# Kernel tuning notes

Measured on AMD Instinct MI355X. Metric: run time of the kernel, lower is better.

Reference implementation:

```python
import jax, jax.numpy as jnp
import numpy as np

WIN = (2, 6, 12)          # (win_Z, win_H, win_W)
HEADS = 6
DIM = 192
IMG = (8, 96, 180)        # (Z, H, W) after patch embedding
NWIN_TOK = WIN[0] * WIN[1] * WIN[2]            # 144 tokens per window
TYPE_W = (IMG[0] // WIN[0]) * (IMG[1] // WIN[1])  # num_Z*num_H = 64
BIAS_ROWS = (2 * WIN[2] - 1) * WIN[1] ** 2 * WIN[0] ** 2  # 3312


def _build_position_index(win):
    wZ, wH, wW = win
    czi = np.arange(wZ); czj = -np.arange(wZ) * wZ
    chi = np.arange(wH); chj = -np.arange(wH) * wH
    cw = np.arange(wW)
    c1 = np.stack(np.meshgrid(czi, chi, cw, indexing='ij'), 0).reshape(3, -1)
    c2 = np.stack(np.meshgrid(czj, chj, cw, indexing='ij'), 0).reshape(3, -1)
    coords = (c1[:, :, None] - c2[:, None, :]).transpose(1, 2, 0).copy()  # (N, N, 3)
    coords[:, :, 2] += wW - 1
    coords[:, :, 1] *= 2 * wW - 1
    coords[:, :, 0] *= (2 * wW - 1) * wH ** 2
    return jnp.asarray(coords.sum(-1).reshape(-1))  # (N*N,) int indices into bias table

POS_IDX = _build_position_index(WIN)


def _layernorm(x, g, b, eps=1e-5):
    m = jnp.mean(x, -1, keepdims=True)
    v = jnp.mean(jnp.square(x - m), -1, keepdims=True)
    return (x - m) * jax.lax.rsqrt(v + eps) * g + b


def setup_inputs() -> dict:
    key = jax.random.key(0)
    ks = jax.random.split(key, 8)
    Z, H, W = IMG
    x = jax.random.normal(ks[0], (1, Z * H * W, DIM), dtype=jnp.float32)
    std = 0.02
    return {
        'x': x,
        'w_qkv': jax.random.normal(ks[1], (DIM, 3 * DIM), dtype=jnp.float32) * std,
        'b_qkv': jnp.zeros((3 * DIM,), jnp.float32),
        'w_proj': jax.random.normal(ks[2], (DIM, DIM), dtype=jnp.float32) * std,
        'b_proj': jnp.zeros((DIM,), jnp.float32),
        'bias_table': jax.random.normal(ks[3], (BIAS_ROWS, TYPE_W, HEADS), dtype=jnp.float32) * std,
        'g1': jnp.ones((DIM,), jnp.float32), 'b1': jnp.zeros((DIM,), jnp.float32),
        'g2': jnp.ones((DIM,), jnp.float32), 'b2': jnp.zeros((DIM,), jnp.float32),
        'w_mlp': jax.random.normal(ks[4], (DIM, DIM), dtype=jnp.float32) * std,
        'b_mlp': jnp.zeros((DIM,), jnp.float32),
        'Z': Z, 'H': H, 'W': W, 'roll': 0,
    }


def reference(x, w_qkv, b_qkv, w_proj, b_proj, bias_table, g1, b1, g2, b2,
              w_mlp, b_mlp, Z, H, W, roll):
    # roll=0 path (is_rolling=False, mask=None), per init_kwargs
    B, T, C = x.shape
    wZ, wH, wW = WIN
    nZ, nH, nW = Z // wZ, H // wH, W // wW
    hd = C // HEADS
    scale = float(hd) ** 0.5
    N = NWIN_TOK

    shortcut = x
    # window partition: (B,Z,H,W,C) -> (B*nZ*nH*nW, N, C)
    xw = (x.reshape(B, nZ, wZ, nH, wH, nW, wW, C)
            .transpose(0, 1, 3, 5, 2, 4, 6, 7)
            .reshape(-1, N, C))
    Bw = xw.shape[0]

    qkv = (xw @ w_qkv + b_qkv).reshape(Bw, N, 3, HEADS, hd).transpose(2, 0, 3, 1, 4)
    q, k, v = qkv[0], qkv[1], qkv[2]                       # (Bw, heads, N, hd)

    attn = jnp.einsum('bhnd,bhmd->bhnm', q, k) / scale     # (Bw, heads, N, N)

    # earth-specific relative position bias: gather then broadcast over f = Bw // TYPE_W
    bias = bias_table[POS_IDX].reshape(N, N, TYPE_W, HEADS).transpose(2, 3, 0, 1)
    f = Bw // TYPE_W
    attn = (attn.reshape(f, TYPE_W, HEADS, N, N) + bias[None]).reshape(Bw, HEADS, N, N)

    attn = jax.nn.softmax(attn, axis=-1)
    out = jnp.einsum('bhnm,bhmd->bhnd', attn, v).transpose(0, 2, 1, 3).reshape(Bw, N, C)
    out = out @ w_proj + b_proj

    # window merge back to (B, Z*H*W, C)
    out = (out.reshape(B, nZ, nH, nW, wZ, wH, wW, C)
              .transpose(0, 1, 4, 2, 5, 3, 6, 7)
              .reshape(B, Z * H * W, C))

    x = shortcut + _layernorm(out, g1, b1)
    x = x + _layernorm(x @ w_mlp + b_mlp, g2, b2)
    return x
```

## Files before the change

kernel.cpp:

```cpp
#include <hip/hip_runtime.h>
#include <hip/hip_bf16.h>


typedef __attribute__((ext_vector_type(8))) short bfrag;
typedef __attribute__((ext_vector_type(4))) float f32x4;
typedef __attribute__((ext_vector_type(4))) unsigned short us4;
typedef __attribute__((ext_vector_type(8))) unsigned short us8;

__device__ __forceinline__ unsigned short f2bf(float f) {
    __hip_bfloat16 h = __float2bfloat16(f);
    unsigned short s;
    __builtin_memcpy(&s, &h, 2);
    return s;
}
__device__ __forceinline__ us4 pack4(float a, float b, float c, float d) {
    us4 o;
    o[0] = f2bf(a); o[1] = f2bf(b); o[2] = f2bf(c); o[3] = f2bf(d);
    return o;
}
__device__ __forceinline__ float bf2f(unsigned short s) {
    return __builtin_bit_cast(float, ((unsigned int)s) << 16);
}
__device__ __forceinline__ int token_of(int iw, int n) {
    int wi = iw % 15, hi = (iw / 15) % 16, zi = iw / 240;
    int ww = n % 12, hh = (n / 12) % 6, zz = n / 72;
    return ((zi * 2 + zz) * 96 + hi * 6 + hh) * 180 + wi * 12 + ww;
}

__global__ __launch_bounds__(256) void wconv(const float* __restrict__ w_qkv,
                                             unsigned short* __restrict__ wt) {
    int id = blockIdx.x * 256 + threadIdx.x;
    if (id >= 110592) return;
    int k = id / 576, c = id - k * 576;
    wt[c * 192 + k] = f2bf(w_qkv[id]);
}

__global__ __launch_bounds__(256) void wconv2(const float* __restrict__ w_proj,
                                              const float* __restrict__ w_mlp,
                                              unsigned short* __restrict__ wp_t,
                                              unsigned short* __restrict__ wm_t) {
    int id = blockIdx.x * 256 + threadIdx.x;
    if (id >= 36864) return;
    const float* src = blockIdx.y ? w_mlp : w_proj;
    unsigned short* dst = blockIdx.y ? wm_t : wp_t;
    int n = id / 192, k = id - n * 192;
    dst[id] = f2bf(src[(size_t)k * 192 + n]);
}

__global__ __launch_bounds__(256) void bias_reorg(const float* __restrict__ bias_table,
                                                  unsigned short* __restrict__ bias_r) {
    __shared__ unsigned short T[384][68];
    int p0 = blockIdx.x * 64;
    int tid = threadIdx.x;
    for (int e = tid; e < 64 * 384; e += 256) {
        int pl = e / 384, th = e - pl * 384;
        int pair = p0 + pl;
        int i = pair / 144, j = pair - i * 144;
        int z1 = i / 72, h1 = (i / 12) % 6, w1 = i % 12;
        int z2 = j / 72, h2 = (j / 12) % 6, w2 = j % 12;
        int idx = (z1 + 2 * z2) * 828 + (h1 + 6 * h2) * 23 + (w1 - w2 + 11);
        T[th][pl] = f2bf(bias_table[(size_t)idx * 384 + th]);
    }
    __syncthreads();
    for (int e = tid; e < 384 * 16; e += 256) {
        int th = e >> 4, pc = e & 15;
        *(us4*)&bias_r[(size_t)th * 20736 + p0 + pc * 4] = *(const us4*)&T[th][pc * 4];
    }
}

__global__ __launch_bounds__(384) void qkattn(const float* __restrict__ x,
                                              const unsigned short* __restrict__ wt,
                                              const float* __restrict__ b_qkv,
                                              const unsigned short* __restrict__ bias_r,
                                              unsigned short* __restrict__ o_ws) {
    __shared__ __align__(16) unsigned short Xw[144 * 200];
    __shared__ __align__(16) unsigned short Ql[2][144 * 40];
    __shared__ __align__(16) unsigned short Kl[2][144 * 40];
    __shared__ __align__(16) unsigned short Vt[2][32 * 168];
    int tid = threadIdx.x;
    int iw = blockIdx.x;
    int w = tid >> 6, l = tid & 63, li = l & 15, lg = l >> 4;
    int tri = w / 3, tw = w - tri * 3;

#pragma unroll
    for (int i = 0; i < 9; ++i) {
        int idx = tid + i * 384;
        int r = idx / 24, g = idx - r * 24;
        const float* xp = &x[(size_t)token_of(iw, r) * 192 + g * 8];
        float4 v0 = *(const float4*)xp;
        float4 v1 = *(const float4*)(xp + 4);
        us4 a = pack4(v0.x, v0.y, v0.z, v0.w);
        us4 b = pack4(v1.x, v1.y, v1.z, v1.w);
        *(us4*)&Xw[r * 200 + g * 8] = a;
        *(us4*)&Xw[r * 200 + g * 8 + 4] = b;
    }
    __syncthreads();

    for (int rnd = 0; rnd < 3; ++rnd) {
        int h = rnd * 2 + tri;

        int wrow = tw * 192 + h * 32;
        f32x4 acc[2][9];
#pragma unroll
        for (int ct = 0; ct < 2; ++ct)
#pragma unroll
            for (int tt = 0; tt < 9; ++tt) acc[ct][tt] = (f32x4){0.f, 0.f, 0.f, 0.f};
        for (int kk = 0; kk < 6; ++kk) {
            int k0 = kk * 32 + lg * 8;
            bfrag wf[2];
#pragma unroll
            for (int ct = 0; ct < 2; ++ct)
                wf[ct] = *(const bfrag*)&wt[(size_t)(wrow + ct * 16 + li) * 192 + k0];
#pragma unroll
            for (int tt = 0; tt < 9; ++tt) {
                bfrag xf = *(const bfrag*)&Xw[(tt * 16 + li) * 200 + k0];
                acc[0][tt] = __builtin_amdgcn_mfma_f32_16x16x32_bf16(wf[0], xf, acc[0][tt], 0, 0, 0);
                acc[1][tt] = __builtin_amdgcn_mfma_f32_16x16x32_bf16(wf[1], xf, acc[1][tt], 0, 0, 0);
            }
        }
        if (tw < 2) {
            unsigned short* dst = (tw == 0) ? &Ql[tri][0] : &Kl[tri][0];
#pragma unroll
            for (int ct = 0; ct < 2; ++ct) {
                float4 bq = *(const float4*)&b_qkv[tw * 192 + h * 32 + ct * 16 + lg * 4];
#pragma unroll
                for (int tt = 0; tt < 9; ++tt) {
                    us4 o = pack4(acc[ct][tt][0] + bq.x, acc[ct][tt][1] + bq.y,
                                  acc[ct][tt][2] + bq.z, acc[ct][tt][3] + bq.w);
                    *(us4*)&dst[(tt * 16 + li) * 40 + ct * 16 + lg * 4] = o;
                }
            }
        } else {
#pragma unroll
            for (int ct = 0; ct < 2; ++ct) {
                float4 bq = *(const float4*)&b_qkv[2 * 192 + h * 32 + ct * 16 + lg * 4];
                float bqa[4] = {bq.x, bq.y, bq.z, bq.w};
#pragma unroll
                for (int tt = 0; tt < 9; ++tt)
#pragma unroll
                    for (int r = 0; r < 4; ++r)
                        Vt[tri][(ct * 16 + lg * 4 + r) * 168 + tt * 16 + li] =
                            f2bf(acc[ct][tt][r] + bqa[r]);
            }
            int d = l >> 1, half = l & 1;
            *(uint4*)&Vt[tri][d * 168 + 144 + half * 8] = (uint4){0u, 0u, 0u, 0u};
        }
        __syncthreads();

        int it0 = tw * 3;
        unsigned short* Pbw = &Ql[tri][(size_t)tw * 48 * 40];
        bfrag qf[3];
#pragma unroll
        for (int itl = 0; itl < 3; ++itl)
            qf[itl] = *(const bfrag*)&Ql[tri][((it0 + itl) * 16 + li) * 40 + lg * 8];

        f32x4 S[9][3];
#pragma unroll
        for (int jt = 0; jt < 9; ++jt) {
            bfrag kf = *(const bfrag*)&Kl[tri][(jt * 16 + li) * 40 + lg * 8];
#pragma unroll
            for (int itl = 0; itl < 3; ++itl) {
                f32x4 z = (f32x4){0.f, 0.f, 0.f, 0.f};
                S[jt][itl] = __builtin_amdgcn_mfma_f32_16x16x32_bf16(kf, qf[itl], z, 0, 0, 0);
            }
        }

        const unsigned short* bp = bias_r + ((size_t)((iw & 63) * 6 + h)) * 20736;
        const float inv_scale = 0.17677669529663687f;
#pragma unroll
        for (int jt = 0; jt < 9; ++jt) {
#pragma unroll
            for (int itl = 0; itl < 3; ++itl) {
                int i = (it0 + itl) * 16 + li;
                int j0 = jt * 16 + lg * 4;
                us4 bv = *(const us4*)&bp[i * 144 + j0];
#pragma unroll
                for (int r = 0; r < 4; ++r)
                    S[jt][itl][r] = S[jt][itl][r] * inv_scale + bf2f(bv[r]);
            }
        }

        float inv[3];
#pragma unroll
        for (int itl = 0; itl < 3; ++itl) {
            float mx = -3.0e38f;
#pragma unroll
            for (int jt = 0; jt < 9; ++jt)
#pragma unroll
                for (int r = 0; r < 4; ++r) mx = fmaxf(mx, S[jt][itl][r]);
            mx = fmaxf(mx, __shfl_xor(mx, 16));
            mx = fmaxf(mx, __shfl_xor(mx, 32));
            float sum = 0.f;
#pragma unroll
            for (int jt = 0; jt < 9; ++jt)
#pragma unroll
                for (int r = 0; r < 4; ++r) {
                    float e = __expf(S[jt][itl][r] - mx);
                    S[jt][itl][r] = e;
                    sum += e;
                }
            sum += __shfl_xor(sum, 16);
            sum += __shfl_xor(sum, 32);
            inv[itl] = 1.f / sum;
        }

        f32x4 O[2][3];
#pragma unroll
        for (int dt = 0; dt < 2; ++dt)
#pragma unroll
            for (int itl = 0; itl < 3; ++itl) O[dt][itl] = (f32x4){0.f, 0.f, 0.f, 0.f};

        for (int jc = 0; jc < 5; ++jc) {
#pragma unroll
            for (int itl = 0; itl < 3; ++itl) {
                int irow = itl * 16 + li;
#pragma unroll
                for (int half = 0; half < 2; ++half) {
                    int jt = jc * 2 + half;
                    us4 pk;
                    if (jt < 9) {
                        pk = pack4(S[jt][itl][0], S[jt][itl][1], S[jt][itl][2], S[jt][itl][3]);
                    } else {
                        pk = (us4){0, 0, 0, 0};
                    }
                    *(us4*)&Pbw[irow * 40 + half * 16 + lg * 4] = pk;
                }
            }
            bfrag pf[3], af[2];
#pragma unroll
            for (int itl = 0; itl < 3; ++itl)
                pf[itl] = *(const bfrag*)&Pbw[(itl * 16 + li) * 40 + lg * 8];
#pragma unroll
            for (int dt = 0; dt < 2; ++dt)
                af[dt] = *(const bfrag*)&Vt[tri][(dt * 16 + li) * 168 + jc * 32 + lg * 8];
#pragma unroll
            for (int dt = 0; dt < 2; ++dt)
#pragma unroll
                for (int itl = 0; itl < 3; ++itl)
                    O[dt][itl] = __builtin_amdgcn_mfma_f32_16x16x32_bf16(af[dt], pf[itl], O[dt][itl], 0, 0, 0);
        }

#pragma unroll
        for (int itl = 0; itl < 3; ++itl) {
#pragma unroll
            for (int dt = 0; dt < 2; ++dt) {
                us4 ov = pack4(O[dt][itl][0] * inv[itl], O[dt][itl][1] * inv[itl],
                               O[dt][itl][2] * inv[itl], O[dt][itl][3] * inv[itl]);
                *(us4*)&Pbw[(itl * 16 + li) * 40 + dt * 16 + lg * 4] = ov;
            }
        }
#pragma unroll
        for (int s = 0; s < 3; ++s) {
            int gi = s * 64 + l;
            int row = gi >> 2, g = gi & 3;
            uint4 v = *(const uint4*)&Pbw[row * 40 + g * 8];
            int t = token_of(iw, it0 * 16 + row);
            *(uint4*)&o_ws[(size_t)t * 192 + h * 32 + g * 8] = v;
        }
        __syncthreads();
    }
}

__global__ __launch_bounds__(512) void mlp_mfma(const unsigned short* __restrict__ o_ws,
                                                const float* __restrict__ x,
                                                const unsigned short* __restrict__ wp_t,
                                                const float* __restrict__ b_proj,
                                                const float* __restrict__ g1,
                                                const float* __restrict__ b1,
                                                const float* __restrict__ g2,
                                                const float* __restrict__ b2,
                                                const unsigned short* __restrict__ wm_t,
                                                const float* __restrict__ b_mlp,
                                                float* __restrict__ out) {
    __shared__ __align__(16) unsigned short Al[128 * 200];
    __shared__ __align__(16) unsigned short Bf[192 * 200];
    int tid = threadIdx.x;
    int t0 = blockIdx.x * 128;
    int w = tid >> 6, l = tid & 63, li = l & 15, lg = l >> 4;

#pragma unroll
    for (int i = 0; i < 9; ++i) {
        int idx = tid + i * 512;
        int r = idx / 24, g = idx - r * 24;
        *(uint4*)&Bf[r * 200 + g * 8] = *(const uint4*)&wp_t[(size_t)r * 192 + g * 8];
    }
    __syncthreads();

    f32x4 C[12];
#pragma unroll
    for (int nt = 0; nt < 12; ++nt) C[nt] = (f32x4){0.f, 0.f, 0.f, 0.f};
    for (int kk = 0; kk < 6; ++kk) {
        int k0 = kk * 32 + lg * 8;
        bfrag a = *(const bfrag*)&o_ws[(size_t)(t0 + w * 16 + li) * 192 + k0];
#pragma unroll
        for (int nt = 0; nt < 12; ++nt) {
            bfrag b = *(const bfrag*)&Bf[(nt * 16 + li) * 200 + k0];
            C[nt] = __builtin_amdgcn_mfma_f32_16x16x32_bf16(a, b, C[nt], 0, 0, 0);
        }
    }
    __syncthreads();

#pragma unroll
    for (int i = 0; i < 9; ++i) {
        int idx = tid + i * 512;
        int r = idx / 24, g = idx - r * 24;
        *(uint4*)&Bf[r * 200 + g * 8] = *(const uint4*)&wm_t[(size_t)r * 192 + g * 8];
    }

    {
        float bp[12], gg[12], bb[12];
#pragma unroll
        for (int nt = 0; nt < 12; ++nt) {
            int f = nt * 16 + li;
            bp[nt] = b_proj[f]; gg[nt] = g1[f]; bb[nt] = b1[f];
        }
#pragma unroll
        for (int r = 0; r < 4; ++r) {
            float s1 = 0.f;
#pragma unroll
            for (int nt = 0; nt < 12; ++nt) s1 += C[nt][r] + bp[nt];
            s1 += __shfl_xor(s1, 1); s1 += __shfl_xor(s1, 2);
            s1 += __shfl_xor(s1, 4); s1 += __shfl_xor(s1, 8);
            float mean = s1 * (1.f / 192.f);
            float s2 = 0.f;
#pragma unroll
            for (int nt = 0; nt < 12; ++nt) {
                float dv = C[nt][r] + bp[nt] - mean; s2 += dv * dv;
            }
            s2 += __shfl_xor(s2, 1); s2 += __shfl_xor(s2, 2);
            s2 += __shfl_xor(s2, 4); s2 += __shfl_xor(s2, 8);
            float rstd = rsqrtf(s2 * (1.f / 192.f) + 1e-5f);
            int row = w * 16 + lg * 4 + r;
            int t = t0 + row;
#pragma unroll
            for (int nt = 0; nt < 12; ++nt) {
                int f = nt * 16 + li;
                float ln = (C[nt][r] + bp[nt] - mean) * rstd * gg[nt] + bb[nt];
                float x1 = x[(size_t)t * 192 + f] + ln;
                C[nt][r] = x1;
                Al[row * 200 + f] = f2bf(x1);
            }
        }
    }
    __syncthreads();

    f32x4 C2[12];
#pragma unroll
    for (int nt = 0; nt < 12; ++nt) C2[nt] = (f32x4){0.f, 0.f, 0.f, 0.f};
    for (int kk = 0; kk < 6; ++kk) {
        int k0 = kk * 32 + lg * 8;
        bfrag a = *(const bfrag*)&Al[(w * 16 + li) * 200 + k0];
#pragma unroll
        for (int nt = 0; nt < 12; ++nt) {
            bfrag b = *(const bfrag*)&Bf[(nt * 16 + li) * 200 + k0];
            C2[nt] = __builtin_amdgcn_mfma_f32_16x16x32_bf16(a, b, C2[nt], 0, 0, 0);
        }
    }

    {
        float bp[12], gg[12], bb[12];
#pragma unroll
        for (int nt = 0; nt < 12; ++nt) {
            int f = nt * 16 + li;
            bp[nt] = b_mlp[f]; gg[nt] = g2[f]; bb[nt] = b2[f];
        }
#pragma unroll
        for (int r = 0; r < 4; ++r) {
            float s1 = 0.f;
#pragma unroll
            for (int nt = 0; nt < 12; ++nt) s1 += C2[nt][r] + bp[nt];
            s1 += __shfl_xor(s1, 1); s1 += __shfl_xor(s1, 2);
            s1 += __shfl_xor(s1, 4); s1 += __shfl_xor(s1, 8);
            float mean = s1 * (1.f / 192.f);
            float s2 = 0.f;
#pragma unroll
            for (int nt = 0; nt < 12; ++nt) {
                float dv = C2[nt][r] + bp[nt] - mean; s2 += dv * dv;
            }
            s2 += __shfl_xor(s2, 1); s2 += __shfl_xor(s2, 2);
            s2 += __shfl_xor(s2, 4); s2 += __shfl_xor(s2, 8);
            float rstd = rsqrtf(s2 * (1.f / 192.f) + 1e-5f);
            int t = t0 + w * 16 + lg * 4 + r;
#pragma unroll
            for (int nt = 0; nt < 12; ++nt) {
                int f = nt * 16 + li;
                float ln = (C2[nt][r] + bp[nt] - mean) * rstd * gg[nt] + bb[nt];
                out[(size_t)t * 192 + f] = C[nt][r] + ln;
            }
        }
    }
}

extern "C" void kernel_launch(void* const* d_in, const int* in_sizes, int n_in,
                              void* d_out, int out_size, void* d_ws, size_t ws_size,
                              hipStream_t stream) {
    const float* x          = (const float*)d_in[0];
    const float* w_qkv      = (const float*)d_in[1];
    const float* b_qkv      = (const float*)d_in[2];
    const float* w_proj     = (const float*)d_in[3];
    const float* b_proj     = (const float*)d_in[4];
    const float* bias_table = (const float*)d_in[5];
    const float* g1         = (const float*)d_in[6];
    const float* b1         = (const float*)d_in[7];
    const float* g2         = (const float*)d_in[8];
    const float* b2         = (const float*)d_in[9];
    const float* w_mlp      = (const float*)d_in[10];
    const float* b_mlp      = (const float*)d_in[11];

    char* ws = (char*)d_ws;
    unsigned short* bias_r = (unsigned short*)ws;
    unsigned short* o_ws   = (unsigned short*)(ws + 15925248);
    unsigned short* w_t    = (unsigned short*)(ws + 69009408);
    unsigned short* wp_t   = (unsigned short*)(ws + 69230592);
    unsigned short* wm_t   = (unsigned short*)(ws + 69304320);

    wconv<<<432, 256, 0, stream>>>(w_qkv, w_t);
    bias_reorg<<<324, 256, 0, stream>>>(bias_table, bias_r);
    qkattn<<<960, 384, 0, stream>>>(x, w_t, b_qkv, bias_r, o_ws);
    wconv2<<<dim3(144, 2), 256, 0, stream>>>(w_proj, w_mlp, wp_t, wm_t);
    mlp_mfma<<<1080, 512, 0, stream>>>(o_ws, x, wp_t, b_proj, g1, b1, g2, b2,
                                       wm_t, b_mlp, (float*)d_out);
}
```

Baseline: 244.1 us.

## Fold softmax scale into Q weights, seed QK MFMA with bias, remap windows

The 1/sqrt(d) scale is folded into the Q columns of the converted QKV weights and into the Q bias, so the score epilogue no longer multiplies by the scale. The relative position bias is loaded directly as the MFMA accumulator input, which fuses the bias add into the QK matmul. Block-to-window mapping is permuted so consecutive blocks spread across Z-slices, which may change L2 locality of the bias table. s_setprio is also placed around the MFMA bursts and the K loop is unrolled. Scaling Q before the bf16 rounding slightly changes numerics.

```diff
diff --git a/kernel.cpp b/kernel.cpp
--- a/kernel.cpp
+++ b/kernel.cpp
@@ -27,12 +27,16 @@
     return ((zi * 2 + zz) * 96 + hi * 6 + hh) * 180 + wi * 12 + ww;
 }
 
+#define INV_SCALE 0.17677669529663687f
+
 __global__ __launch_bounds__(256) void wconv(const float* __restrict__ w_qkv,
                                              unsigned short* __restrict__ wt) {
     int id = blockIdx.x * 256 + threadIdx.x;
     if (id >= 110592) return;
     int k = id / 576, c = id - k * 576;
-    wt[c * 192 + k] = f2bf(w_qkv[id]);
+    float v = w_qkv[id];
+    if (c < 192) v *= INV_SCALE;
+    wt[c * 192 + k] = f2bf(v);
 }
 
 __global__ __launch_bounds__(256) void wconv2(const float* __restrict__ w_proj,
@@ -78,7 +82,7 @@
     __shared__ __align__(16) unsigned short Kl[2][144 * 40];
     __shared__ __align__(16) unsigned short Vt[2][32 * 168];
     int tid = threadIdx.x;
-    int iw = blockIdx.x;
+    int iw = (blockIdx.x & 7) * 120 + (blockIdx.x >> 3);
     int w = tid >> 6, l = tid & 63, li = l & 15, lg = l >> 4;
     int tri = w / 3, tw = w - tri * 3;
 
@@ -105,24 +109,29 @@
         for (int ct = 0; ct < 2; ++ct)
 #pragma unroll
             for (int tt = 0; tt < 9; ++tt) acc[ct][tt] = (f32x4){0.f, 0.f, 0.f, 0.f};
+#pragma unroll
         for (int kk = 0; kk < 6; ++kk) {
             int k0 = kk * 32 + lg * 8;
             bfrag wf[2];
 #pragma unroll
             for (int ct = 0; ct < 2; ++ct)
                 wf[ct] = *(const bfrag*)&wt[(size_t)(wrow + ct * 16 + li) * 192 + k0];
+            __builtin_amdgcn_s_setprio(1);
 #pragma unroll
             for (int tt = 0; tt < 9; ++tt) {
                 bfrag xf = *(const bfrag*)&Xw[(tt * 16 + li) * 200 + k0];
                 acc[0][tt] = __builtin_amdgcn_mfma_f32_16x16x32_bf16(wf[0], xf, acc[0][tt], 0, 0, 0);
                 acc[1][tt] = __builtin_amdgcn_mfma_f32_16x16x32_bf16(wf[1], xf, acc[1][tt], 0, 0, 0);
             }
+            __builtin_amdgcn_s_setprio(0);
         }
         if (tw < 2) {
             unsigned short* dst = (tw == 0) ? &Ql[tri][0] : &Kl[tri][0];
+            float bscale = (tw == 0) ? INV_SCALE : 1.0f;
 #pragma unroll
             for (int ct = 0; ct < 2; ++ct) {
                 float4 bq = *(const float4*)&b_qkv[tw * 192 + h * 32 + ct * 16 + lg * 4];
+                bq.x *= bscale; bq.y *= bscale; bq.z *= bscale; bq.w *= bscale;
 #pragma unroll
                 for (int tt = 0; tt < 9; ++tt) {
                     us4 o = pack4(acc[ct][tt][0] + bq.x, acc[ct][tt][1] + bq.y,
@@ -154,30 +163,23 @@
         for (int itl = 0; itl < 3; ++itl)
             qf[itl] = *(const bfrag*)&Ql[tri][((it0 + itl) * 16 + li) * 40 + lg * 8];
 
+        const unsigned short* bp = bias_r + ((size_t)((iw & 63) * 6 + h)) * 20736;
         f32x4 S[9][3];
 #pragma unroll
         for (int jt = 0; jt < 9; ++jt) {
             bfrag kf = *(const bfrag*)&Kl[tri][(jt * 16 + li) * 40 + lg * 8];
-#pragma unroll
-            for (int itl = 0; itl < 3; ++itl) {
-                f32x4 z = (f32x4){0.f, 0.f, 0.f, 0.f};
-                S[jt][itl] = __builtin_amdgcn_mfma_f32_16x16x32_bf16(kf, qf[itl], z, 0, 0, 0);
-            }
-        }
-
-        const unsigned short* bp = bias_r + ((size_t)((iw & 63) * 6 + h)) * 20736;
-        const float inv_scale = 0.17677669529663687f;
-#pragma unroll
-        for (int jt = 0; jt < 9; ++jt) {
+            __builtin_amdgcn_s_setprio(1);
 #pragma unroll
             for (int itl = 0; itl < 3; ++itl) {
                 int i = (it0 + itl) * 16 + li;
                 int j0 = jt * 16 + lg * 4;
                 us4 bv = *(const us4*)&bp[i * 144 + j0];
-#pragma unroll
-                for (int r = 0; r < 4; ++r)
-                    S[jt][itl][r] = S[jt][itl][r] * inv_scale + bf2f(bv[r]);
-            }
+                f32x4 c;
+                c[0] = bf2f(bv[0]); c[1] = bf2f(bv[1]);
+                c[2] = bf2f(bv[2]); c[3] = bf2f(bv[3]);
+                S[jt][itl] = __builtin_amdgcn_mfma_f32_16x16x32_bf16(kf, qf[itl], c, 0, 0, 0);
+            }
+            __builtin_amdgcn_s_setprio(0);
         }
 
         float inv[3];
@@ -233,11 +235,13 @@
 #pragma unroll
             for (int dt = 0; dt < 2; ++dt)
                 af[dt] = *(const bfrag*)&Vt[tri][(dt * 16 + li) * 168 + jc * 32 + lg * 8];
+            __builtin_amdgcn_s_setprio(1);
 #pragma unroll
             for (int dt = 0; dt < 2; ++dt)
 #pragma unroll
                 for (int itl = 0; itl < 3; ++itl)
                     O[dt][itl] = __builtin_amdgcn_mfma_f32_16x16x32_bf16(af[dt], pf[itl], O[dt][itl], 0, 0, 0);
+            __builtin_amdgcn_s_setprio(0);
         }
 
 #pragma unroll
```

Result: slower. 265.3 us (+8.7%).
